# Performance work log

Measured on AMD Instinct MI355X. Metric: run time of the kernel, lower is better.

The kernel has to match this reference:

```python
import jax, jax.numpy as jnp
import numpy as np
import math

IN_FEATURES = 2048
OUT_FEATURES = 8192


def setup_inputs() -> dict:
    key = jax.random.key(0)
    kx, kw = jax.random.split(key)
    x = jax.random.normal(kx, (4, 2048, IN_FEATURES), dtype=jnp.float32)
    stdv = 1.0 / math.sqrt(IN_FEATURES)
    weight = jax.random.uniform(kw, (OUT_FEATURES, IN_FEATURES), dtype=jnp.float32,
                                minval=-stdv, maxval=stdv)
    return {"x": x, "weight": weight}


def reference(x, weight):
    # absmean-based adjustment factor (BitNet b1.58 style)
    scale = 0.0001 + jnp.mean(jnp.abs(weight))
    adjusted = weight / scale
    # two_bit quantization: round then clip to {-1, 0, 1}
    q = jnp.clip(jnp.round(adjusted), -1.0, 1.0)
    # scaled dense matmul: out[b,s,o] = scale * sum_i x[b,s,i] * q[o,i]
    out = scale * jnp.einsum('bsi,oi->bso', x, q)
    return out
```

## Files before the change

### kernel.cpp

```cpp
#include <hip/hip_runtime.h>
#include <hip/hip_bf16.h>


typedef __bf16 bf16x8 __attribute__((ext_vector_type(8)));
typedef float  f32x4  __attribute__((ext_vector_type(4)));

#define GAS __attribute__((address_space(1)))
#define LAS __attribute__((address_space(3)))

static constexpr int  M_DIM = 8192;
static constexpr int  N_DIM = 8192;
static constexpr int  K_DIM = 2048;
static constexpr long NELEM = 16777216;

__global__ void absmean1_kernel(const float* __restrict__ w, double* __restrict__ partials) {
    double s = 0.0;
    const float4* w4 = (const float4*)w;
    const int n4 = (int)(NELEM / 4);
    for (int i = blockIdx.x * blockDim.x + threadIdx.x; i < n4; i += gridDim.x * blockDim.x) {
        float4 v = w4[i];
        s += (double)fabsf(v.x) + (double)fabsf(v.y) + (double)fabsf(v.z) + (double)fabsf(v.w);
    }
    #pragma unroll
    for (int off = 32; off > 0; off >>= 1) s += __shfl_down(s, off);
    __shared__ double wsum[4];
    if ((threadIdx.x & 63) == 0) wsum[threadIdx.x >> 6] = s;
    __syncthreads();
    if (threadIdx.x == 0) partials[blockIdx.x] = wsum[0] + wsum[1] + wsum[2] + wsum[3];
}

__global__ void absmean2_kernel(const double* __restrict__ partials, float* __restrict__ scale_out) {
    double s = 0.0;
    #pragma unroll
    for (int j = 0; j < 8; ++j) s += partials[threadIdx.x + 256 * j];
    #pragma unroll
    for (int off = 32; off > 0; off >>= 1) s += __shfl_down(s, off);
    __shared__ double wsum[4];
    if ((threadIdx.x & 63) == 0) wsum[threadIdx.x >> 6] = s;
    __syncthreads();
    if (threadIdx.x == 0) {
        double total = wsum[0] + wsum[1] + wsum[2] + wsum[3];
        scale_out[0] = (float)(1.0e-4 + total * (1.0 / 16777216.0));
    }
}

__global__ void prep_kernel(const float* __restrict__ x, const float* __restrict__ w,
                            const float* __restrict__ scale_in,
                            __bf16* __restrict__ xs, __bf16* __restrict__ qw) {
    const float scale = scale_in[0];
    const int n8 = (int)(NELEM / 8);
    const float4* x4 = (const float4*)x;
    const float4* w4 = (const float4*)w;
    for (int i = blockIdx.x * blockDim.x + threadIdx.x; i < n8; i += gridDim.x * blockDim.x) {
        float4 a0 = x4[2 * i], a1 = x4[2 * i + 1];
        bf16x8 xv;
        xv[0] = (__bf16)(a0.x * scale); xv[1] = (__bf16)(a0.y * scale);
        xv[2] = (__bf16)(a0.z * scale); xv[3] = (__bf16)(a0.w * scale);
        xv[4] = (__bf16)(a1.x * scale); xv[5] = (__bf16)(a1.y * scale);
        xv[6] = (__bf16)(a1.z * scale); xv[7] = (__bf16)(a1.w * scale);
        *(bf16x8*)(xs + 8l * i) = xv;

        float4 b0 = w4[2 * i], b1 = w4[2 * i + 1];
        float wv[8] = {b0.x, b0.y, b0.z, b0.w, b1.x, b1.y, b1.z, b1.w};
        bf16x8 qv;
        #pragma unroll
        for (int e = 0; e < 8; ++e) {
            float r = rintf(wv[e] / scale);
            r = fminf(1.0f, fmaxf(-1.0f, r));
            qv[e] = (__bf16)r;
        }
        *(bf16x8*)(qw + 8l * i) = qv;
    }
}

__global__ __launch_bounds__(256, 2) void gemm_kernel(const __bf16* __restrict__ A,
                                                      const __bf16* __restrict__ B,
                                                      float* __restrict__ C) {
    __shared__ __bf16 As[128 * 64];
    __shared__ __bf16 Bs[128 * 64];

    const int tid  = threadIdx.x;
    const int lane = tid & 63;
    const int wid  = tid >> 6;
    const int wr   = wid >> 1;
    const int wc   = wid & 1;

    const int linear = blockIdx.y * gridDim.x + blockIdx.x;
    const int swzid  = (linear & 7) * 512 + (linear >> 3);
    const int bm = swzid >> 6;
    const int bn = swzid & 63;

    const int lrow   = lane >> 3;
    const int lchunk = lane & 7;
    const int schunk = lchunk ^ lrow;

    const long a_row0 = (long)bm * 128 + wid * 32 + lrow;
    const long b_row0 = (long)bn * 128 + wid * 32 + lrow;

    f32x4 acc[4][4];
    #pragma unroll
    for (int i = 0; i < 4; ++i)
        #pragma unroll
        for (int j = 0; j < 4; ++j)
            acc[i][j] = f32x4{0.0f, 0.0f, 0.0f, 0.0f};

    const char* As_c = (const char*)As;
    const char* Bs_c = (const char*)Bs;
    const int frow_a = wr * 64 + (lane & 15);
    const int frow_b = wc * 64 + (lane & 15);
    const int fcolb  = (lane >> 4) << 4;
    const int swz    = (lane & 7) << 4;

    for (int kt = 0; kt < K_DIM / 64; ++kt) {
        const int k0 = kt * 64;
        #pragma unroll
        for (int i = 0; i < 4; ++i) {
            const __bf16* ga = A + (a_row0 + i * 8) * K_DIM + k0 + schunk * 8;
            __builtin_amdgcn_global_load_lds((const GAS unsigned int*)ga,
                (LAS unsigned int*)(As + (wid * 32 + i * 8) * 64), 16, 0, 0);
            const __bf16* gb = B + (b_row0 + i * 8) * K_DIM + k0 + schunk * 8;
            __builtin_amdgcn_global_load_lds((const GAS unsigned int*)gb,
                (LAS unsigned int*)(Bs + (wid * 32 + i * 8) * 64), 16, 0, 0);
        }
        __syncthreads();

        #pragma unroll
        for (int kk = 0; kk < 2; ++kk) {
            bf16x8 af[4], bg[4];
            #pragma unroll
            for (int i = 0; i < 4; ++i)
                af[i] = *(const bf16x8*)(As_c + (frow_a + i * 16) * 128 + ((fcolb | (kk << 6)) ^ swz));
            #pragma unroll
            for (int j = 0; j < 4; ++j)
                bg[j] = *(const bf16x8*)(Bs_c + (frow_b + j * 16) * 128 + ((fcolb | (kk << 6)) ^ swz));
            #pragma unroll
            for (int i = 0; i < 4; ++i)
                #pragma unroll
                for (int j = 0; j < 4; ++j)
                    acc[i][j] = __builtin_amdgcn_mfma_f32_16x16x32_bf16(af[i], bg[j], acc[i][j], 0, 0, 0);
        }
        __syncthreads();
    }

    const int crow = (lane >> 4) * 4;
    const int ccol = lane & 15;
    #pragma unroll
    for (int i = 0; i < 4; ++i) {
        #pragma unroll
        for (int j = 0; j < 4; ++j) {
            #pragma unroll
            for (int r = 0; r < 4; ++r) {
                const long gm = (long)bm * 128 + wr * 64 + i * 16 + crow + r;
                const long gn = (long)bn * 128 + wc * 64 + j * 16 + ccol;
                C[gm * N_DIM + gn] = acc[i][j][r];
            }
        }
    }
}

extern "C" void kernel_launch(void* const* d_in, const int* in_sizes, int n_in,
                              void* d_out, int out_size, void* d_ws, size_t ws_size,
                              hipStream_t stream) {
    const float* x = (const float*)d_in[0];
    const float* w = (const float*)d_in[1];
    float* out = (float*)d_out;

    char* ws = (char*)d_ws;
    __bf16* qw = (__bf16*)ws;
    __bf16* xs = (__bf16*)(ws + 33554432);

    char* tail = (char*)d_out + (size_t)out_size * sizeof(float);
    double* partials = (double*)(tail - 16384);
    float* scalep    = (float*)(tail - 16448);

    absmean1_kernel<<<2048, 256, 0, stream>>>(w, partials);
    absmean2_kernel<<<1, 256, 0, stream>>>(partials, scalep);
    prep_kernel<<<2048, 256, 0, stream>>>(x, w, scalep, xs, qw);
    dim3 grid(N_DIM / 128, M_DIM / 128);
    gemm_kernel<<<grid, 256, 0, stream>>>(xs, qw, out);
}
```

Baseline: 647.5 us.

## Restructure GEMM into 256x256 tiles with double-buffered LDS and phased prefetch

The bf16 GEMM moves from 128x128 tiles with 4 waves to 256x256 tiles with 8 waves. It double-buffers 128 KB of LDS and splits each K-step into eight quarter-tile phases, each of which issues the next stage's global-to-LDS loads while MFMAs run. Manual waitcnt, barriers and setprio control the overlap of memory and compute. The aim is to hide global load latency and raise arithmetic intensity per LDS byte. The costs are higher register pressure (128 accumulator floats per thread), fragile hand-written synchronization, and lower occupancy, since 128 KB of LDS may allow only one block per CU.

```diff
diff --git a/kernel.cpp b/kernel.cpp
--- a/kernel.cpp
+++ b/kernel.cpp
@@ -73,86 +73,115 @@
     }
 }
 
-__global__ __launch_bounds__(256, 2) void gemm_kernel(const __bf16* __restrict__ A,
+
+#define STAGE_A(dd, t, kt) do { \
+    _Pragma("unroll") for (int _h = 0; _h < 2; ++_h) { \
+        const __bf16* _g = A + (long)(bm * 256 + _h * 128 + (t) * 64 + (tid >> 3)) * K_DIM \
+                             + (kt) * 64 + schunk * 8; \
+        __builtin_amdgcn_global_load_lds((const GAS unsigned int*)_g, \
+            (LAS unsigned int*)(lds + (dd) * 32768 + _h * 8192 + (t) * 4096 + wid * 512), 16, 0, 0); \
+    } } while (0)
+
+#define STAGE_B(dd, h, kt) do { \
+    _Pragma("unroll") for (int _t = 0; _t < 2; ++_t) { \
+        const __bf16* _g = B + (long)(bn * 256 + (h) * 128 + _t * 64 + (tid >> 3)) * K_DIM \
+                             + (kt) * 64 + schunk * 8; \
+        __builtin_amdgcn_global_load_lds((const GAS unsigned int*)_g, \
+            (LAS unsigned int*)(lds + (dd) * 32768 + 16384 + (h) * 8192 + _t * 4096 + wid * 512), 16, 0, 0); \
+    } } while (0)
+
+#define VM2 asm volatile("s_waitcnt vmcnt(2)" ::: "memory")
+
+#define PHASE(dd, mq, nq, STG, DOVM) do { \
+    bf16x8 af[4][2], bg[2][2]; \
+    _Pragma("unroll") for (int mi = 0; mi < 4; ++mi) \
+        _Pragma("unroll") for (int kk = 0; kk < 2; ++kk) \
+            af[mi][kk] = *(const bf16x8*)(L + (dd) * 65536 \
+                + (wr * 128 + (mq) * 64 + mi * 16 + l15) * 128 + (kk ? kb1 : kb0)); \
+    _Pragma("unroll") for (int nj = 0; nj < 2; ++nj) \
+        _Pragma("unroll") for (int kk = 0; kk < 2; ++kk) \
+            bg[nj][kk] = *(const bf16x8*)(L + (dd) * 65536 + 32768 \
+                + (wc * 64 + (nq) * 32 + nj * 16 + l15) * 128 + (kk ? kb1 : kb0)); \
+    STG; \
+    __builtin_amdgcn_s_barrier(); \
+    asm volatile("s_waitcnt lgkmcnt(0)" ::: "memory"); \
+    __builtin_amdgcn_sched_barrier(0); \
+    __builtin_amdgcn_s_setprio(1); \
+    _Pragma("unroll") for (int mi = 0; mi < 4; ++mi) \
+        _Pragma("unroll") for (int nj = 0; nj < 2; ++nj) \
+            _Pragma("unroll") for (int kk = 0; kk < 2; ++kk) \
+                acc[(mq) * 4 + mi][(nq) * 2 + nj] = __builtin_amdgcn_mfma_f32_16x16x32_bf16( \
+                    af[mi][kk], bg[nj][kk], acc[(mq) * 4 + mi][(nq) * 2 + nj], 0, 0, 0); \
+    __builtin_amdgcn_s_setprio(0); \
+    DOVM; \
+    __builtin_amdgcn_s_barrier(); \
+} while (0)
+
+__global__ __launch_bounds__(512, 2) void gemm_kernel(const __bf16* __restrict__ A,
                                                       const __bf16* __restrict__ B,
                                                       float* __restrict__ C) {
-    __shared__ __bf16 As[128 * 64];
-    __shared__ __bf16 Bs[128 * 64];
+    __shared__ __bf16 lds[65536];
 
     const int tid  = threadIdx.x;
     const int lane = tid & 63;
     const int wid  = tid >> 6;
-    const int wr   = wid >> 1;
-    const int wc   = wid & 1;
+    const int wr   = wid >> 2;
+    const int wc   = wid & 3;
+    const int l15  = lane & 15;
 
     const int linear = blockIdx.y * gridDim.x + blockIdx.x;
-    const int swzid  = (linear & 7) * 512 + (linear >> 3);
-    const int bm = swzid >> 6;
-    const int bn = swzid & 63;
-
-    const int lrow   = lane >> 3;
-    const int lchunk = lane & 7;
-    const int schunk = lchunk ^ lrow;
-
-    const long a_row0 = (long)bm * 128 + wid * 32 + lrow;
-    const long b_row0 = (long)bn * 128 + wid * 32 + lrow;
-
-    f32x4 acc[4][4];
-    #pragma unroll
-    for (int i = 0; i < 4; ++i)
+    const int swzid  = (linear & 7) * 128 + (linear >> 3);
+    const int bm = swzid >> 5;
+    const int bn = swzid & 31;
+
+    const int schunk = (tid & 7) ^ ((tid >> 3) & 7);
+
+    const int swz = (lane & 7) << 4;
+    const int khi = ((lane >> 4) & 3) << 4;
+    const int kb0 = khi ^ swz;
+    const int kb1 = (khi | 64) ^ swz;
+    const char* L = (const char*)lds;
+
+    f32x4 acc[8][4];
+    #pragma unroll
+    for (int i = 0; i < 8; ++i)
         #pragma unroll
         for (int j = 0; j < 4; ++j)
             acc[i][j] = f32x4{0.0f, 0.0f, 0.0f, 0.0f};
 
-    const char* As_c = (const char*)As;
-    const char* Bs_c = (const char*)Bs;
-    const int frow_a = wr * 64 + (lane & 15);
-    const int frow_b = wc * 64 + (lane & 15);
-    const int fcolb  = (lane >> 4) << 4;
-    const int swz    = (lane & 7) << 4;
-
-    for (int kt = 0; kt < K_DIM / 64; ++kt) {
-        const int k0 = kt * 64;
+    STAGE_A(0, 0, 0);
+    STAGE_A(0, 1, 0);
+    STAGE_B(0, 0, 0);
+    STAGE_B(0, 1, 0);
+    STAGE_A(1, 0, 1);
+    VM2;
+    __builtin_amdgcn_s_barrier();
+
+    const int NITER = K_DIM / 128;
+    for (int i = 0; i < NITER; ++i) {
+        const int kt1 = 2 * i + 1;
+        const int kt2 = (2 * i + 2) & 31;
+        const int kt3 = (2 * i + 3) & 31;
+        PHASE(0, 0, 0, STAGE_A(1, 1, kt1), );
+        PHASE(0, 1, 0, STAGE_B(1, 0, kt1), );
+        PHASE(0, 0, 1, STAGE_B(1, 1, kt1), );
+        PHASE(0, 1, 1, STAGE_A(0, 0, kt2), VM2);
+        PHASE(1, 0, 0, STAGE_B(0, 0, kt2), );
+        PHASE(1, 1, 0, STAGE_B(0, 1, kt2), );
+        PHASE(1, 0, 1, STAGE_A(0, 1, kt2), );
+        PHASE(1, 1, 1, STAGE_A(1, 0, kt3), VM2);
+    }
+
+    const int crow = (lane >> 4) << 2;
+    #pragma unroll
+    for (int mi = 0; mi < 8; ++mi) {
         #pragma unroll
-        for (int i = 0; i < 4; ++i) {
-            const __bf16* ga = A + (a_row0 + i * 8) * K_DIM + k0 + schunk * 8;
-            __builtin_amdgcn_global_load_lds((const GAS unsigned int*)ga,
-                (LAS unsigned int*)(As + (wid * 32 + i * 8) * 64), 16, 0, 0);
-            const __bf16* gb = B + (b_row0 + i * 8) * K_DIM + k0 + schunk * 8;
-            __builtin_amdgcn_global_load_lds((const GAS unsigned int*)gb,
-                (LAS unsigned int*)(Bs + (wid * 32 + i * 8) * 64), 16, 0, 0);
-        }
-        __syncthreads();
-
-        #pragma unroll
-        for (int kk = 0; kk < 2; ++kk) {
-            bf16x8 af[4], bg[4];
-            #pragma unroll
-            for (int i = 0; i < 4; ++i)
-                af[i] = *(const bf16x8*)(As_c + (frow_a + i * 16) * 128 + ((fcolb | (kk << 6)) ^ swz));
-            #pragma unroll
-            for (int j = 0; j < 4; ++j)
-                bg[j] = *(const bf16x8*)(Bs_c + (frow_b + j * 16) * 128 + ((fcolb | (kk << 6)) ^ swz));
-            #pragma unroll
-            for (int i = 0; i < 4; ++i)
-                #pragma unroll
-                for (int j = 0; j < 4; ++j)
-                    acc[i][j] = __builtin_amdgcn_mfma_f32_16x16x32_bf16(af[i], bg[j], acc[i][j], 0, 0, 0);
-        }
-        __syncthreads();
-    }
-
-    const int crow = (lane >> 4) * 4;
-    const int ccol = lane & 15;
-    #pragma unroll
-    for (int i = 0; i < 4; ++i) {
-        #pragma unroll
-        for (int j = 0; j < 4; ++j) {
+        for (int nj = 0; nj < 4; ++nj) {
             #pragma unroll
             for (int r = 0; r < 4; ++r) {
-                const long gm = (long)bm * 128 + wr * 64 + i * 16 + crow + r;
-                const long gn = (long)bn * 128 + wc * 64 + j * 16 + ccol;
-                C[gm * N_DIM + gn] = acc[i][j][r];
+                const long gm = (long)bm * 256 + wr * 128 + mi * 16 + crow + r;
+                const long gn = (long)bn * 256 + wc * 64 + nj * 16 + l15;
+                C[gm * N_DIM + gn] = acc[mi][nj][r];
             }
         }
     }
@@ -176,6 +205,6 @@
     absmean1_kernel<<<2048, 256, 0, stream>>>(w, partials);
     absmean2_kernel<<<1, 256, 0, stream>>>(partials, scalep);
     prep_kernel<<<2048, 256, 0, stream>>>(x, w, scalep, xs, qw);
-    dim3 grid(N_DIM / 128, M_DIM / 128);
-    gemm_kernel<<<grid, 256, 0, stream>>>(xs, qw, out);
-}
+    dim3 grid(32, 32);
+    gemm_kernel<<<grid, 512, 0, stream>>>(xs, qw, out);
+}
```

Measured after the change: 582.0 us. 10.1% less time.
